# Kernel optimization log

Hardware: AMD Instinct MI355X
Metric: run time of the kernel (lower is better)

Reference implementation:

```python
import jax, jax.numpy as jnp
from jax import lax
import numpy as np

H_FEAT = 14
W_FEAT = 14
BN_EPS = 1e-5
NORM_EPS = 1e-12

def _coord_tensor():
    # Python-2 integer division as in the original repo
    c = np.zeros((H_FEAT * W_FEAT, 2), dtype=np.float32)
    for i in range(H_FEAT * W_FEAT):
        c[i, 0] = (i // W_FEAT - H_FEAT // 2) / (H_FEAT / 2.0)
        c[i, 1] = (i % W_FEAT - W_FEAT // 2) / (W_FEAT / 2.0)
    return jnp.asarray(c.reshape(1, H_FEAT, W_FEAT, 2).transpose(0, 3, 1, 2))  # [1,2,14,14]

def _l2norm(x, axis):
    n = jnp.linalg.norm(x, axis=axis, keepdims=True)
    return x / jnp.maximum(n, NORM_EPS)

def _conv2d(x, w, b, pad):
    y = lax.conv_general_dilated(x, w, (1, 1), [(pad, pad), (pad, pad)],
                                 dimension_numbers=("NCHW", "OIHW", "NCHW"))
    return y + b[None, :, None, None]

def _bn_train(x, g, b):
    m = x.mean(axis=(0, 2, 3), keepdims=True)
    v = x.var(axis=(0, 2, 3), keepdims=True)
    return (x - m) * lax.rsqrt(v + BN_EPS) * g[None, :, None, None] + b[None, :, None, None]

def _lstm_scan(emb, Wih, Whh, bih, bhh):
    # emb: [T, B, 300]; PyTorch gate order i,f,g,o
    Hdim = Whh.shape[1]
    B = emb.shape[1]
    def step(carry, x):
        h, c = carry
        gates = x @ Wih.T + h @ Whh.T + bih + bhh  # [B, 4H]
        i, f, g, o = jnp.split(gates, 4, axis=-1)
        c = jax.nn.sigmoid(f) * c + jax.nn.sigmoid(i) * jnp.tanh(g)
        h = jax.nn.sigmoid(o) * jnp.tanh(c)
        return (h, c), h
    init = (jnp.zeros((B, Hdim), emb.dtype), jnp.zeros((B, Hdim), emb.dtype))
    _, hs = lax.scan(step, init, emb)
    return hs  # [T, B, H]

def _resblock(v, coord, c1w, c1b, c2w, c2b, bng, bnb):
    B = v.shape[0]
    vin = jnp.concatenate([v, jnp.broadcast_to(coord, (B, 2, H_FEAT, W_FEAT))], axis=1)
    v1 = jax.nn.relu(_conv2d(vin, c1w, c1b, 0))
    v2 = jax.nn.relu(_bn_train(_conv2d(v1, c2w, c2b, 1), bng, bnb))
    return v2 + v1

def setup_inputs() -> dict:
    key = jax.random.key(0)
    ks = jax.random.split(key, 24)
    B, T, V, E = 128, 45, 10000, 300
    Hh = 1024
    s = 0.02
    inp = {}
    inp["que"] = jax.random.randint(ks[0], (B, T), 0, V, dtype=jnp.int64)
    inp["img"] = jax.random.normal(ks[1], (B, 1024, H_FEAT, W_FEAT), dtype=jnp.float32)
    inp["lookup"] = s * jax.random.normal(ks[2], (V + 1, E), dtype=jnp.float32)
    inp["Wih_f"] = s * jax.random.normal(ks[3], (4 * Hh, E), dtype=jnp.float32)
    inp["Whh_f"] = s * jax.random.normal(ks[4], (4 * Hh, Hh), dtype=jnp.float32)
    inp["bih_f"] = jnp.zeros((4 * Hh,), jnp.float32)
    inp["bhh_f"] = jnp.zeros((4 * Hh,), jnp.float32)
    inp["Wih_b"] = s * jax.random.normal(ks[5], (4 * Hh, E), dtype=jnp.float32)
    inp["Whh_b"] = s * jax.random.normal(ks[6], (4 * Hh, Hh), dtype=jnp.float32)
    inp["bih_b"] = jnp.zeros((4 * Hh,), jnp.float32)
    inp["bhh_b"] = jnp.zeros((4 * Hh,), jnp.float32)
    inp["conv0_w"] = s * jax.random.normal(ks[7], (128, 1026, 3, 3), dtype=jnp.float32)
    inp["conv0_b"] = jnp.zeros((128,), jnp.float32)
    inp["bn0_g"] = jnp.ones((128,), jnp.float32)
    inp["bn0_b"] = jnp.zeros((128,), jnp.float32)
    inp["r1c1_w"] = s * jax.random.normal(ks[8], (128, 130, 1, 1), dtype=jnp.float32)
    inp["r1c1_b"] = jnp.zeros((128,), jnp.float32)
    inp["r1c2_w"] = s * jax.random.normal(ks[9], (128, 128, 3, 3), dtype=jnp.float32)
    inp["r1c2_b"] = jnp.zeros((128,), jnp.float32)
    inp["r1bn_g"] = jnp.ones((128,), jnp.float32)
    inp["r1bn_b"] = jnp.zeros((128,), jnp.float32)
    inp["r2c1_w"] = s * jax.random.normal(ks[10], (128, 130, 1, 1), dtype=jnp.float32)
    inp["r2c1_b"] = jnp.zeros((128,), jnp.float32)
    inp["r2c2_w"] = s * jax.random.normal(ks[11], (128, 128, 3, 3), dtype=jnp.float32)
    inp["r2c2_b"] = jnp.zeros((128,), jnp.float32)
    inp["r2bn_g"] = jnp.ones((128,), jnp.float32)
    inp["r2bn_b"] = jnp.zeros((128,), jnp.float32)
    return inp

def reference(que, img, lookup, Wih_f, Whh_f, bih_f, bhh_f, Wih_b, Whh_b, bih_b, bhh_b,
              conv0_w, conv0_b, bn0_g, bn0_b,
              r1c1_w, r1c1_b, r1c2_w, r1c2_b, r1bn_g, r1bn_b,
              r2c1_w, r2c1_b, r2c2_w, r2c2_b, r2bn_g, r2bn_b):
    coord = _coord_tensor()
    # ---- encoder (LSTM mode) ----
    emb = lookup[que]                      # [B, T, 300]
    emb = jnp.transpose(emb, (1, 0, 2))    # [T, B, 300]
    h_f = _lstm_scan(emb, Wih_f, Whh_f, bih_f, bhh_f)
    h_b = _lstm_scan(emb[::-1], Wih_b, Whh_b, bih_b, bhh_b)[::-1]
    qenc = _l2norm(jnp.concatenate([h_f, h_b], axis=-1), axis=-1)  # [T, B, 2048]
    enc = qenc[-1]                                                  # [B, 2048]
    # ---- image branch ----
    v = _l2norm(img, axis=1)               # per-pixel L2 norm over 1024 channels
    B = v.shape[0]
    v = jnp.concatenate([v, jnp.broadcast_to(coord, (B, 2, H_FEAT, W_FEAT))], axis=1)
    v = jax.nn.relu(_bn_train(_conv2d(v, conv0_w, conv0_b, 1), bn0_g, bn0_b))
    v = _resblock(v, coord, r1c1_w, r1c1_b, r1c2_w, r1c2_b, r1bn_g, r1bn_b)
    v = _resblock(v, coord, r2c1_w, r2c1_b, r2c2_w, r2c2_b, r2bn_g, r2bn_b)
    return (enc, v)
```

## Files before the change

### kernel.cpp

```cpp
#include <hip/hip_runtime.h>
#include <math.h>

#define BB   128
#define T    45
#define E    300
#define HH   1024
#define G4   4096
#define HW   196
#define NPX  (BB*HW)
#define C0   1026
#define CM   128
#define CR   130
#define TCH  15

static __device__ __forceinline__ float sigm(float x) { return 1.f / (1.f + __expf(-x)); }

__global__ void k_embed(const int* __restrict__ que, const float* __restrict__ lookup,
                        float* __restrict__ emb) {
    int idx = blockIdx.x * 256 + threadIdx.x;
    if (idx >= T * BB * E) return;
    int e = idx % E;
    int n = idx / E;
    int b = n % BB;
    int t = n / BB;
    int q = que[b * T + t];
    emb[idx] = lookup[(size_t)q * E + e];
}

template <int BM, int BN, int TM, int TN>
__global__ __launch_bounds__(256) void k_gemm_nt(
    const float* __restrict__ A, int lda,
    const float* __restrict__ Bw, int ldb,
    const float* __restrict__ add,
    const float* __restrict__ bias,
    float* __restrict__ C, int ldc,
    int M, int N, int K, int relu) {
    constexpr int KT = 16;
    constexpr int TX = BN / TN;
    __shared__ float As[KT][BM + 4];
    __shared__ float Bs[KT][BN + 4];
    const int tid = threadIdx.x;
    const int tx = tid % TX, ty = tid / TX;
    const int r0 = blockIdx.x * BM, c0 = blockIdx.y * BN;
    float acc[TM][TN] = {};
    for (int k0 = 0; k0 < K; k0 += KT) {
#pragma unroll
        for (int l = tid; l < BM * KT; l += 256) {
            int m = l / KT, k = l % KT;
            int gm = r0 + m, gk = k0 + k;
            As[k][m] = (gm < M && gk < K) ? A[(size_t)gm * lda + gk] : 0.f;
        }
#pragma unroll
        for (int l = tid; l < BN * KT; l += 256) {
            int n = l / KT, k = l % KT;
            int gn = c0 + n, gk = k0 + k;
            Bs[k][n] = (gn < N && gk < K) ? Bw[(size_t)gn * ldb + gk] : 0.f;
        }
        __syncthreads();
#pragma unroll
        for (int k = 0; k < KT; ++k) {
            float ar[TM], br[TN];
#pragma unroll
            for (int i = 0; i < TM; ++i) ar[i] = As[k][ty * TM + i];
#pragma unroll
            for (int j = 0; j < TN; ++j) br[j] = Bs[k][tx * TN + j];
#pragma unroll
            for (int i = 0; i < TM; ++i)
#pragma unroll
                for (int j = 0; j < TN; ++j) acc[i][j] += ar[i] * br[j];
        }
        __syncthreads();
    }
#pragma unroll
    for (int i = 0; i < TM; ++i) {
        int gm = r0 + ty * TM + i;
        if (gm >= M) continue;
#pragma unroll
        for (int j = 0; j < TN; ++j) {
            int gn = c0 + tx * TN + j;
            if (gn >= N) continue;
            float v = acc[i][j];
            if (add) v += add[(size_t)gm * ldc + gn];
            if (bias) v += bias[gn];
            if (relu) v = fmaxf(v, 0.f);
            C[(size_t)gm * ldc + gn] = v;
        }
    }
}

__global__ void k_pack_wih(const float* __restrict__ Wih, float* __restrict__ o) {
    int idx = blockIdx.x * 256 + threadIdx.x;
    if (idx >= G4 * E) return;
    int k = idx % E;
    int n = idx / E;
    o[idx] = Wih[(size_t)((n & 3) * HH + (n >> 2)) * E + k];
}
__global__ void k_pack_whh(const float* __restrict__ Whh, float* __restrict__ o) {
    int idx = blockIdx.x * 256 + threadIdx.x;
    if (idx >= G4 * HH) return;
    int k = idx & 1023;
    int n = idx >> 10;
    o[idx] = Whh[(size_t)((n & 3) * HH + (n >> 2)) * HH + k];
}
__global__ void k_pack_b4i(const float* __restrict__ bih, const float* __restrict__ bhh,
                           float* __restrict__ out) {
    int n = blockIdx.x * 256 + threadIdx.x;
    if (n >= G4) return;
    int r = (n & 3) * HH + (n >> 2);
    out[n] = bih[r] + bhh[r];
}
__global__ void k_biasadd(const float* __restrict__ bih, const float* __restrict__ bhh,
                          float* __restrict__ out) {
    int idx = blockIdx.x * 256 + threadIdx.x;
    if (idx < G4) out[idx] = bih[idx] + bhh[idx];
}

__global__ void k_cell_plain(float* __restrict__ h, float* __restrict__ c,
                             const float* __restrict__ gx, int first) {
    int idx = blockIdx.x * 256 + threadIdx.x;
    int b = idx >> 10, j = idx & 1023;
    size_t base = (size_t)b * G4 + j;
    float gi = gx[base], gf = gx[base + HH], gg = gx[base + 2 * HH], go = gx[base + 3 * HH];
    float cp = first ? 0.f : c[idx];
    float cn = sigm(gf) * cp + sigm(gi) * tanhf(gg);
    c[idx] = cn;
    h[idx] = sigm(go) * tanhf(cn);
}

__global__ __launch_bounds__(256) void k_lstm_fused(
    const float* __restrict__ h_in, float* __restrict__ c_io,
    const float* __restrict__ gx,
    const float* __restrict__ Wpk,
    float* __restrict__ h_out, int first) {
    __shared__ float As[16][36];
    __shared__ float Bs[16][68];
    const int tid = threadIdx.x;
    const int tx = tid & 15, ty = tid >> 4;
    const int r0 = blockIdx.x * 32;
    const int c0 = blockIdx.y * 64;
    const int ka = tid & 15, ma = tid >> 4;
    float acc[2][4] = {};

#define LSTM_LD(K0)                                                               \
    {                                                                             \
        int gk = (K0) + ka;                                                       \
        rA0 = h_in[(size_t)(r0 + ma) * HH + gk];                                  \
        rA1 = h_in[(size_t)(r0 + ma + 16) * HH + gk];                             \
        const float* wp = Wpk + (size_t)(c0 + ma) * HH + gk;                      \
        rB0 = wp[0];                                                              \
        rB1 = wp[(size_t)16 * HH];                                                \
        rB2 = wp[(size_t)32 * HH];                                                \
        rB3 = wp[(size_t)48 * HH];                                                \
    }

    if (!first) {
        float rA0, rA1, rB0, rB1, rB2, rB3;
        LSTM_LD(0);
        for (int k0 = 0; k0 < HH; k0 += 16) {
            As[ka][ma] = rA0;
            As[ka][ma + 16] = rA1;
            Bs[ka][ma] = rB0;
            Bs[ka][ma + 16] = rB1;
            Bs[ka][ma + 32] = rB2;
            Bs[ka][ma + 48] = rB3;
            __syncthreads();
            if (k0 + 16 < HH) LSTM_LD(k0 + 16);
#pragma unroll
            for (int k = 0; k < 16; ++k) {
                float a0 = As[k][ty * 2], a1 = As[k][ty * 2 + 1];
                float br[4];
#pragma unroll
                for (int j = 0; j < 4; ++j) br[j] = Bs[k][tx * 4 + j];
#pragma unroll
                for (int j = 0; j < 4; ++j) {
                    acc[0][j] += a0 * br[j];
                    acc[1][j] += a1 * br[j];
                }
            }
            __syncthreads();
        }
    }
#undef LSTM_LD
    const int jj4 = c0 + tx * 4;
    const int u = jj4 >> 2;
#pragma unroll
    for (int i = 0; i < 2; ++i) {
        int b = r0 + ty * 2 + i;
        float4 g4 = *(const float4*)&gx[(size_t)b * G4 + jj4];
        float gi = acc[i][0] + g4.x;
        float gf = acc[i][1] + g4.y;
        float gg = acc[i][2] + g4.z;
        float go = acc[i][3] + g4.w;
        size_t ci = (size_t)b * HH + u;
        float cp = first ? 0.f : c_io[ci];
        float cn = sigm(gf) * cp + sigm(gi) * tanhf(gg);
        c_io[ci] = cn;
        h_out[ci] = sigm(go) * tanhf(cn);
    }
}

__global__ void k_enc(const float* __restrict__ hf, const float* __restrict__ hb,
                      float* __restrict__ out) {
    int b = blockIdx.x;
    int tid = threadIdx.x;
    float vals[8];
    float ss = 0.f;
#pragma unroll
    for (int i = 0; i < 8; ++i) {
        int j = i * 256 + tid;
        float v = (j < HH) ? hf[(size_t)b * HH + j] : hb[(size_t)b * HH + (j - HH)];
        vals[i] = v;
        ss += v * v;
    }
    __shared__ float red[256];
    red[tid] = ss;
    __syncthreads();
    for (int s = 128; s > 0; s >>= 1) {
        if (tid < s) red[tid] += red[tid + s];
        __syncthreads();
    }
    float scale = 1.f / fmaxf(sqrtf(red[0]), 1e-12f);
#pragma unroll
    for (int i = 0; i < 8; ++i) out[(size_t)b * 2048 + i * 256 + tid] = vals[i] * scale;
}

__global__ void k_pixssq(const float* __restrict__ img, float* __restrict__ ssq) {
    int b = blockIdx.x >> 4;
    int cc = (blockIdx.x & 15) * 64;
    int p = threadIdx.x;
    if (p >= HW) return;
    const float* base = img + ((size_t)b * 1024 + cc) * HW + p;
    float acc = 0.f;
#pragma unroll 4
    for (int c = 0; c < 64; ++c) {
        float v = base[(size_t)c * HW];
        acc += v * v;
    }
    atomicAdd(&ssq[b * HW + p], acc);
}

__global__ void k_invn(float* __restrict__ ssq) {
    int i = blockIdx.x * 256 + threadIdx.x;
    if (i >= NPX) return;
    ssq[i] = 1.f / fmaxf(sqrtf(ssq[i]), 1e-12f);
}

__global__ void k_packB0(const float* __restrict__ w, float* __restrict__ o) {
    int idx = blockIdx.x * 256 + threadIdx.x;
    if (idx >= 8 * 9 * 1040 * 16) return;
    int oi = idx & 15;
    int r = idx >> 4;
    int c = r % 1040;
    int gt = r / 1040;
    int tap = gt % 9, ocg = gt / 9;
    o[idx] = (c < C0) ? w[((size_t)(ocg * 16 + oi) * C0 + c) * 9 + tap] : 0.f;
}
__global__ void k_packBpm(const float* __restrict__ w, float* __restrict__ o) {
    int idx = blockIdx.x * 256 + threadIdx.x;
    if (idx >= 8 * 9 * 128 * 16) return;
    int oi = idx & 15;
    int r = idx >> 4;
    int c = r % 128;
    int gt = r / 128;
    int tap = gt % 9, ocg = gt / 9;
    o[idx] = w[((size_t)(ocg * 16 + oi) * 128 + c) * 9 + tap];
}

static __device__ __forceinline__ void conv_swizzle(int id, int& g, int& ocg, int& z) {
    int x = id & 7, q = id >> 3;
    int cb;
    if (q < 192) { g = ((q >> 4) << 3) + x; cb = q & 15; }
    else { int r = ((q - 192) << 3) + x; g = 96 + (r >> 4); cb = r & 15; }
    ocg = cb >> 1;
    z = cb & 1;
}

__global__ __launch_bounds__(256) void k_conv0(const float* __restrict__ img,
                                               const float* __restrict__ invn,
                                               const float* __restrict__ wpk,
                                               const float* __restrict__ bias,
                                               float* __restrict__ outParts) {
    __shared__ float As[289][20];
    const int tid = threadIdx.x;
    int g, ocg, z;
    conv_swizzle(blockIdx.x, g, ocg, z);
    const int kbeg = z ? 528 : 0;
    const int kend = z ? 1040 : 528;
    float* out = outParts + (size_t)z * NPX * CM;
    const int P0 = g * 256;
    const int gpix = P0 + tid;
    const int p = gpix % HW;
    const int y = p / 14, x = p % 14;
    float acc[16] = {};
    if (tid < 16) As[288][tid] = 0.f;
    for (int k0 = kbeg; k0 < kend; k0 += 16) {
        __syncthreads();
        for (int l = tid; l < 288 * 16; l += 256) {
            int s = l >> 4, k = l & 15;
            int gp = P0 - 16 + s;
            float v = 0.f;
            if (gp >= 0 && gp < NPX) {
                int gk = k0 + k;
                int pp = gp % HW;
                int bi = gp / HW;
                if (gk < 1024) v = img[((size_t)bi * 1024 + gk) * HW + pp] * invn[gp];
                else if (gk == 1024) v = (float)(pp / 14 - 7) * (1.f / 7.f);
                else if (gk == 1025) v = (float)(pp % 14 - 7) * (1.f / 7.f);
            }
            As[s][k] = v;
        }
        __syncthreads();
        for (int tap = 0; tap < 9; ++tap) {
            const int ky = tap / 3 - 1, kx = tap % 3 - 1;
            const int yy = y + ky, xx = x + kx;
            const int of = ((unsigned)yy < 14u && (unsigned)xx < 14u)
                               ? (tid + 16 + ky * 14 + kx) : 288;
            const float4* __restrict__ wq =
                (const float4*)wpk + ((size_t)(ocg * 9 + tap) * 1040 + k0) * 4;
            for (int kq = 0; kq < 4; ++kq) {
                float4 a4 = *(const float4*)&As[of][kq * 4];
                float av[4] = {a4.x, a4.y, a4.z, a4.w};
#pragma unroll
                for (int kk = 0; kk < 4; ++kk) {
                    float a = av[kk];
                    float4 w0 = wq[0], w1 = wq[1], w2 = wq[2], w3 = wq[3];
                    wq += 4;
                    acc[0]  += a * w0.x;  acc[1]  += a * w0.y;
                    acc[2]  += a * w0.z;  acc[3]  += a * w0.w;
                    acc[4]  += a * w1.x;  acc[5]  += a * w1.y;
                    acc[6]  += a * w1.z;  acc[7]  += a * w1.w;
                    acc[8]  += a * w2.x;  acc[9]  += a * w2.y;
                    acc[10] += a * w2.z;  acc[11] += a * w2.w;
                    acc[12] += a * w3.x;  acc[13] += a * w3.y;
                    acc[14] += a * w3.z;  acc[15] += a * w3.w;
                }
            }
        }
    }
    float* op = out + (size_t)gpix * CM + ocg * 16;
    const float* bp = bias + ocg * 16;
#pragma unroll
    for (int qq = 0; qq < 4; ++qq) {
        float4 r;
        r.x = acc[qq * 4 + 0] + (z ? 0.f : bp[qq * 4 + 0]);
        r.y = acc[qq * 4 + 1] + (z ? 0.f : bp[qq * 4 + 1]);
        r.z = acc[qq * 4 + 2] + (z ? 0.f : bp[qq * 4 + 2]);
        r.w = acc[qq * 4 + 3] + (z ? 0.f : bp[qq * 4 + 3]);
        *(float4*)&op[qq * 4] = r;
    }
}

__global__ __launch_bounds__(256) void k_conv_pm(const float* __restrict__ vin,
                                                 const float* __restrict__ wpk,
                                                 const float* __restrict__ bias,
                                                 float* __restrict__ outParts) {
    __shared__ float As[289][20];
    const int tid = threadIdx.x;
    int g, ocg, z;
    conv_swizzle(blockIdx.x, g, ocg, z);
    const int kbeg = z * 64;
    float* out = outParts + (size_t)z * NPX * CM;
    const int P0 = g * 256;
    const int gpix = P0 + tid;
    const int p = gpix % HW;
    const int y = p / 14, x = p % 14;
    float acc[16] = {};
    if (tid < 16) As[288][tid] = 0.f;
    for (int k0 = kbeg; k0 < kbeg + 64; k0 += 16) {
        __syncthreads();
        for (int l = tid; l < 288 * 4; l += 256) {
            int s = l >> 2, kq = l & 3;
            int gp = P0 - 16 + s;
            float4 v;
            v.x = v.y = v.z = v.w = 0.f;
            if (gp >= 0 && gp < NPX) v = *(const float4*)&vin[(size_t)gp * CM + k0 + kq * 4];
            *(float4*)&As[s][kq * 4] = v;
        }
        __syncthreads();
        for (int tap = 0; tap < 9; ++tap) {
            const int ky = tap / 3 - 1, kx = tap % 3 - 1;
            const int yy = y + ky, xx = x + kx;
            const int of = ((unsigned)yy < 14u && (unsigned)xx < 14u)
                               ? (tid + 16 + ky * 14 + kx) : 288;
            const float4* __restrict__ wq =
                (const float4*)wpk + ((size_t)(ocg * 9 + tap) * 128 + k0) * 4;
            for (int kq = 0; kq < 4; ++kq) {
                float4 a4 = *(const float4*)&As[of][kq * 4];
                float av[4] = {a4.x, a4.y, a4.z, a4.w};
#pragma unroll
                for (int kk = 0; kk < 4; ++kk) {
                    float a = av[kk];
                    float4 w0 = wq[0], w1 = wq[1], w2 = wq[2], w3 = wq[3];
                    wq += 4;
                    acc[0]  += a * w0.x;  acc[1]  += a * w0.y;
                    acc[2]  += a * w0.z;  acc[3]  += a * w0.w;
                    acc[4]  += a * w1.x;  acc[5]  += a * w1.y;
                    acc[6]  += a * w1.z;  acc[7]  += a * w1.w;
                    acc[8]  += a * w2.x;  acc[9]  += a * w2.y;
                    acc[10] += a * w2.z;  acc[11] += a * w2.w;
                    acc[12] += a * w3.x;  acc[13] += a * w3.y;
                    acc[14] += a * w3.z;  acc[15] += a * w3.w;
                }
            }
        }
    }
    float* op = out + (size_t)gpix * CM + ocg * 16;
    const float* bp = bias + ocg * 16;
#pragma unroll
    for (int qq = 0; qq < 4; ++qq) {
        float4 r;
        r.x = acc[qq * 4 + 0] + (z ? 0.f : bp[qq * 4 + 0]);
        r.y = acc[qq * 4 + 1] + (z ? 0.f : bp[qq * 4 + 1]);
        r.z = acc[qq * 4 + 2] + (z ? 0.f : bp[qq * 4 + 2]);
        r.w = acc[qq * 4 + 3] + (z ? 0.f : bp[qq * 4 + 3]);
        *(float4*)&op[qq * 4] = r;
    }
}

__global__ void k_bnstats(const float* __restrict__ xa, const float* __restrict__ xb,
                          float* __restrict__ stats) {
    int r0 = blockIdx.x * 224;
    int c = threadIdx.x & 127, rh = threadIdx.x >> 7;
    float s = 0.f, ss = 0.f;
    for (int r = r0 + rh; r < r0 + 224; r += 2) {
        float v = xa[(size_t)r * CM + c] + xb[(size_t)r * CM + c];
        s += v;
        ss += v * v;
    }
    __shared__ float rs[256], rss[256];
    rs[threadIdx.x] = s;
    rss[threadIdx.x] = ss;
    __syncthreads();
    if (threadIdx.x < 128) {
        s = rs[threadIdx.x] + rs[threadIdx.x + 128];
        ss = rss[threadIdx.x] + rss[threadIdx.x + 128];
        atomicAdd(&stats[c], s);
        atomicAdd(&stats[128 + c], ss);
    }
}

__global__ void k_bnfinal(const float* __restrict__ stats, const float* __restrict__ g,
                          const float* __restrict__ b, float* __restrict__ scsh) {
    int c = threadIdx.x;
    if (c >= 128) return;
    float mean = stats[c] / (float)NPX;
    float var = stats[128 + c] / (float)NPX - mean * mean;
    float sc = g[c] * rsqrtf(var + 1e-5f);
    scsh[c] = sc;
    scsh[128 + c] = b[c] - mean * sc;
}

__global__ void k_apply_cat(const float* __restrict__ xa, const float* __restrict__ xb,
                            const float* __restrict__ scsh,
                            const float* __restrict__ addv, float* __restrict__ vinr) {
    int idx = blockIdx.x * 256 + threadIdx.x;
    if (idx >= NPX * CM) return;
    int c = idx & 127;
    int p = idx >> 7;
    float v = fmaxf((xa[idx] + xb[idx]) * scsh[c] + scsh[128 + c], 0.f);
    if (addv) v += addv[idx];
    vinr[(size_t)p * CR + c] = v;
}

__global__ void k_coords_r(float* __restrict__ vinr) {
    int p = blockIdx.x * 256 + threadIdx.x;
    if (p >= NPX) return;
    int pp = p % HW;
    int y = pp / 14, x = pp % 14;
    vinr[(size_t)p * CR + 128] = (float)(y - 7) * (1.f / 7.f);
    vinr[(size_t)p * CR + 129] = (float)(x - 7) * (1.f / 7.f);
}

__global__ void k_final(const float* __restrict__ xa, const float* __restrict__ xb,
                        const float* __restrict__ scsh,
                        const float* __restrict__ addv, float* __restrict__ outv) {
    int idx = blockIdx.x * 256 + threadIdx.x;
    if (idx >= NPX * CM) return;
    int p = idx % HW;
    int o = (idx / HW) & 127;
    int b = idx / (HW * CM);
    size_t pm = ((size_t)b * HW + p) * CM + o;
    outv[idx] = fmaxf((xa[pm] + xb[pm]) * scsh[o] + scsh[128 + o], 0.f) + addv[pm];
}

extern "C" void kernel_launch(void* const* d_in, const int* in_sizes, int n_in,
                              void* d_out, int out_size, void* d_ws, size_t ws_size,
                              hipStream_t stream) {
    const int* que = (const int*)d_in[0];
    const float* img = (const float*)d_in[1];
    const float* lookup = (const float*)d_in[2];
    const float* Wih_f = (const float*)d_in[3];
    const float* Whh_f = (const float*)d_in[4];
    const float* bih_f = (const float*)d_in[5];
    const float* bhh_f = (const float*)d_in[6];
    const float* Wih_b = (const float*)d_in[7];
    const float* bih_b = (const float*)d_in[9];
    const float* bhh_b = (const float*)d_in[10];
    const float* conv0_w = (const float*)d_in[11];
    const float* conv0_b = (const float*)d_in[12];
    const float* bn0_g = (const float*)d_in[13];
    const float* bn0_b = (const float*)d_in[14];
    const float* r1c1_w = (const float*)d_in[15];
    const float* r1c1_b = (const float*)d_in[16];
    const float* r1c2_w = (const float*)d_in[17];
    const float* r1c2_b = (const float*)d_in[18];
    const float* r1bn_g = (const float*)d_in[19];
    const float* r1bn_b = (const float*)d_in[20];
    const float* r2c1_w = (const float*)d_in[21];
    const float* r2c1_b = (const float*)d_in[22];
    const float* r2c2_w = (const float*)d_in[23];
    const float* r2c2_b = (const float*)d_in[24];
    const float* r2bn_g = (const float*)d_in[25];
    const float* r2bn_b = (const float*)d_in[26];
    float* out = (float*)d_out;

    float* ws = (float*)d_ws;
    float* emb = ws;
    float* Xg = emb + 1728000;
    float* WihPk = Xg + 7864320;
    float* WhhPk = WihPk + 1228800;
    float* b4i = WhhPk + 4194304;
    float* b4b = b4i + 4096;
    float* Xb = b4b + 4096;
    float* hA = Xb + 524288;
    float* hB = hA + 131072;
    float* cbuf = hB + 131072;
    float* hbb = cbuf + 131072;
    size_t lstm_end = (size_t)(hbb + 131072 - ws);
    float* invn = ws;
    float* wpk0 = invn + 25088;
    float* wpk1 = wpk0 + 1198080;
    float* wpk2 = wpk1 + 147456;
    float* xa = wpk2 + 147456;
    float* xb = xa + 3211264;
    float* vinr = xb + 3211264;
    float* v1 = vinr + 3261440;
    float* stats = v1 + 3211264;
    float* scsh = stats + 256;
    size_t img_end = (size_t)(scsh + 256 - ws);
    size_t need = (lstm_end > img_end ? lstm_end : img_end) * 4;
    if (ws_size < need) return;

    auto cdiv = [](int a, int b) { return (a + b - 1) / b; };
    const size_t BG = (size_t)BB * G4;

    k_embed<<<cdiv(T * BB * E, 256), 256, 0, stream>>>(que, lookup, emb);
    k_pack_wih<<<cdiv(G4 * E, 256), 256, 0, stream>>>(Wih_f, WihPk);
    k_pack_whh<<<cdiv(G4 * HH, 256), 256, 0, stream>>>(Whh_f, WhhPk);
    k_pack_b4i<<<16, 256, 0, stream>>>(bih_f, bhh_f, b4i);
    k_biasadd<<<16, 256, 0, stream>>>(bih_b, bhh_b, b4b);
    k_gemm_nt<64, 64, 4, 4><<<dim3(2, 64), 256, 0, stream>>>(
        emb + (size_t)(T - 1) * BB * E, E, Wih_b, E, nullptr, b4b, Xb, G4, BB, G4, E, 0);
    k_cell_plain<<<512, 256, 0, stream>>>(hbb, cbuf, Xb, 1);
    float* hp = hA;
    float* hq = hB;
    float* hlast = hA;
    for (int ch = 0; ch < 3; ++ch) {
        int t0 = ch * TCH;
        k_gemm_nt<64, 64, 4, 4><<<dim3(30, 64), 256, 0, stream>>>(
            emb + (size_t)t0 * BB * E, E, WihPk, E, nullptr, b4i, Xg, G4,
            TCH * BB, G4, E, 0);
        for (int s = 0; s < TCH; ++s) {
            int t = t0 + s;
            k_lstm_fused<<<dim3(4, 64), 256, 0, stream>>>(
                hq, cbuf, Xg + (size_t)s * BG, WhhPk, hp, (t == 0) ? 1 : 0);
            hlast = hp;
            float* tmp = hp; hp = hq; hq = tmp;
        }
    }
    k_enc<<<128, 256, 0, stream>>>(hlast, hbb, out);

    hipMemsetAsync(invn, 0, NPX * 4, stream);
    k_pixssq<<<BB * 16, 256, 0, stream>>>(img, invn);
    k_invn<<<cdiv(NPX, 256), 256, 0, stream>>>(invn);
    k_packB0<<<cdiv(8 * 9 * 1040 * 16, 256), 256, 0, stream>>>(conv0_w, wpk0);
    k_packBpm<<<cdiv(8 * 9 * 128 * 16, 256), 256, 0, stream>>>(r1c2_w, wpk1);
    k_packBpm<<<cdiv(8 * 9 * 128 * 16, 256), 256, 0, stream>>>(r2c2_w, wpk2);

    k_conv0<<<1568, 256, 0, stream>>>(img, invn, wpk0, conv0_b, xa);
    hipMemsetAsync(stats, 0, 256 * 4, stream);
    k_bnstats<<<112, 256, 0, stream>>>(xa, xb, stats);
    k_bnfinal<<<1, 128, 0, stream>>>(stats, bn0_g, bn0_b, scsh);
    k_apply_cat<<<cdiv(NPX * CM, 256), 256, 0, stream>>>(xa, xb, scsh, nullptr, vinr);
    k_coords_r<<<cdiv(NPX, 256), 256, 0, stream>>>(vinr);

    k_gemm_nt<64, 64, 4, 4><<<dim3(392, 2), 256, 0, stream>>>(
        vinr, CR, r1c1_w, CR, nullptr, r1c1_b, v1, CM, NPX, CM, CR, 1);
    k_conv_pm<<<1568, 256, 0, stream>>>(v1, wpk1, r1c2_b, xa);
    hipMemsetAsync(stats, 0, 256 * 4, stream);
    k_bnstats<<<112, 256, 0, stream>>>(xa, xb, stats);
    k_bnfinal<<<1, 128, 0, stream>>>(stats, r1bn_g, r1bn_b, scsh);
    k_apply_cat<<<cdiv(NPX * CM, 256), 256, 0, stream>>>(xa, xb, scsh, v1, vinr);

    k_gemm_nt<64, 64, 4, 4><<<dim3(392, 2), 256, 0, stream>>>(
        vinr, CR, r2c1_w, CR, nullptr, r2c1_b, v1, CM, NPX, CM, CR, 1);
    k_conv_pm<<<1568, 256, 0, stream>>>(v1, wpk2, r2c2_b, xa);
    hipMemsetAsync(stats, 0, 256 * 4, stream);
    k_bnstats<<<112, 256, 0, stream>>>(xa, xb, stats);
    k_bnfinal<<<1, 128, 0, stream>>>(stats, r2bn_g, r2bn_b, scsh);
    k_final<<<cdiv(NPX * CM, 256), 256, 0, stream>>>(xa, xb, scsh, v1, out + (size_t)BB * 2048);
}
```

Measured before the change: 4.254 ms.

## Compute two pixels per thread in 3x3 conv kernels to reuse weight loads

Each thread in the conv0 and residual 3x3 conv kernels now accumulates two pixels, with 512 pixels per block instead of 256. The grid is halved and uses a new block swizzle. Every weight float4 loaded from global memory now feeds twice as many FMAs, which cuts weight-read traffic per output. conv0 also precomputes per-thread image pointers and inverse norms and stages the image slab with strided loads. The costs are double the accumulator registers, a larger shared tile with an 18-float padded stride read as float2, fewer blocks per launch, and possible occupancy loss.

```diff
diff --git a/kernel.cpp b/kernel.cpp
--- a/kernel.cpp
+++ b/kernel.cpp
@@ -266,11 +266,10 @@
     o[idx] = w[((size_t)(ocg * 16 + oi) * 128 + c) * 9 + tap];
 }
 
-static __device__ __forceinline__ void conv_swizzle(int id, int& g, int& ocg, int& z) {
-    int x = id & 7, q = id >> 3;
-    int cb;
-    if (q < 192) { g = ((q >> 4) << 3) + x; cb = q & 15; }
-    else { int r = ((q - 192) << 3) + x; g = 96 + (r >> 4); cb = r & 15; }
+static __device__ __forceinline__ void conv_swz784(int id, int& g, int& ocg, int& z) {
+    int s2 = (id & 7) * 98 + (id >> 3);
+    g = s2 >> 4;
+    int cb = s2 & 15;
     ocg = cb >> 1;
     z = cb & 1;
 }
@@ -280,73 +279,122 @@
                                                const float* __restrict__ wpk,
                                                const float* __restrict__ bias,
                                                float* __restrict__ outParts) {
-    __shared__ float As[289][20];
+    __shared__ float As[545][18];
     const int tid = threadIdx.x;
     int g, ocg, z;
-    conv_swizzle(blockIdx.x, g, ocg, z);
+    conv_swz784(blockIdx.x, g, ocg, z);
     const int kbeg = z ? 528 : 0;
     const int kend = z ? 1040 : 528;
     float* out = outParts + (size_t)z * NPX * CM;
-    const int P0 = g * 256;
-    const int gpix = P0 + tid;
-    const int p = gpix % HW;
-    const int y = p / 14, x = p % 14;
-    float acc[16] = {};
-    if (tid < 16) As[288][tid] = 0.f;
+    const int P0 = g * 512;
+    const int gp1 = P0 + tid;
+    const int gp2 = gp1 + 256;
+    const int p1 = gp1 % HW, p2 = gp2 % HW;
+    const int y1 = p1 / 14, x1 = p1 % 14;
+    const int y2 = p2 / 14, x2 = p2 % 14;
+
+    const float* sptr[3];
+    float sinv[3], scy[3], scx[3];
+#pragma unroll
+    for (int j = 0; j < 3; ++j) {
+        int s = tid + j * 256;
+        int gp = P0 - 16 + s;
+        bool ok = (s <= 542) && (gp >= 0) && (gp < NPX);
+        int gpc = ok ? gp : 0;
+        int pp = gpc % HW;
+        int bi = gpc / HW;
+        sptr[j] = img + ((size_t)bi * 1024) * HW + pp;
+        sinv[j] = ok ? invn[gpc] : 0.f;
+        scy[j] = ok ? (float)(pp / 14 - 7) * (1.f / 7.f) : 0.f;
+        scx[j] = ok ? (float)(pp % 14 - 7) * (1.f / 7.f) : 0.f;
+    }
+
+    float acc0[16] = {};
+    float acc1[16] = {};
     for (int k0 = kbeg; k0 < kend; k0 += 16) {
         __syncthreads();
-        for (int l = tid; l < 288 * 16; l += 256) {
-            int s = l >> 4, k = l & 15;
-            int gp = P0 - 16 + s;
-            float v = 0.f;
-            if (gp >= 0 && gp < NPX) {
-                int gk = k0 + k;
-                int pp = gp % HW;
-                int bi = gp / HW;
-                if (gk < 1024) v = img[((size_t)bi * 1024 + gk) * HW + pp] * invn[gp];
-                else if (gk == 1024) v = (float)(pp / 14 - 7) * (1.f / 7.f);
-                else if (gk == 1025) v = (float)(pp % 14 - 7) * (1.f / 7.f);
+        if (k0 < 1024) {
+#pragma unroll
+            for (int j = 0; j < 3; ++j) {
+                int s = tid + j * 256;
+                if (j < 2 || s < 545) {
+                    const float* pbase = sptr[j] + (size_t)k0 * HW;
+                    float inv = sinv[j];
+#pragma unroll
+                    for (int k = 0; k < 16; ++k) As[s][k] = pbase[(size_t)k * HW] * inv;
+                }
             }
-            As[s][k] = v;
+        } else {
+#pragma unroll
+            for (int j = 0; j < 3; ++j) {
+                int s = tid + j * 256;
+                if (j < 2 || s < 545) {
+                    As[s][0] = scy[j];
+                    As[s][1] = scx[j];
+#pragma unroll
+                    for (int k = 2; k < 16; ++k) As[s][k] = 0.f;
+                }
+            }
         }
         __syncthreads();
         for (int tap = 0; tap < 9; ++tap) {
             const int ky = tap / 3 - 1, kx = tap % 3 - 1;
-            const int yy = y + ky, xx = x + kx;
-            const int of = ((unsigned)yy < 14u && (unsigned)xx < 14u)
-                               ? (tid + 16 + ky * 14 + kx) : 288;
+            const int d = ky * 14 + kx;
+            const int of1 = ((unsigned)(y1 + ky) < 14u && (unsigned)(x1 + kx) < 14u)
+                                ? (tid + 16 + d) : 544;
+            const int of2 = ((unsigned)(y2 + ky) < 14u && (unsigned)(x2 + kx) < 14u)
+                                ? (tid + 272 + d) : 544;
             const float4* __restrict__ wq =
                 (const float4*)wpk + ((size_t)(ocg * 9 + tap) * 1040 + k0) * 4;
+#pragma unroll
             for (int kq = 0; kq < 4; ++kq) {
-                float4 a4 = *(const float4*)&As[of][kq * 4];
-                float av[4] = {a4.x, a4.y, a4.z, a4.w};
+                float2 a01 = *(const float2*)&As[of1][kq * 4];
+                float2 a23 = *(const float2*)&As[of1][kq * 4 + 2];
+                float2 b01 = *(const float2*)&As[of2][kq * 4];
+                float2 b23 = *(const float2*)&As[of2][kq * 4 + 2];
+                float av[4] = {a01.x, a01.y, a23.x, a23.y};
+                float bv[4] = {b01.x, b01.y, b23.x, b23.y};
 #pragma unroll
                 for (int kk = 0; kk < 4; ++kk) {
-                    float a = av[kk];
+                    float a = av[kk], b = bv[kk];
                     float4 w0 = wq[0], w1 = wq[1], w2 = wq[2], w3 = wq[3];
                     wq += 4;
-                    acc[0]  += a * w0.x;  acc[1]  += a * w0.y;
-                    acc[2]  += a * w0.z;  acc[3]  += a * w0.w;
-                    acc[4]  += a * w1.x;  acc[5]  += a * w1.y;
-                    acc[6]  += a * w1.z;  acc[7]  += a * w1.w;
-                    acc[8]  += a * w2.x;  acc[9]  += a * w2.y;
-                    acc[10] += a * w2.z;  acc[11] += a * w2.w;
-                    acc[12] += a * w3.x;  acc[13] += a * w3.y;
-                    acc[14] += a * w3.z;  acc[15] += a * w3.w;
+                    acc0[0]  += a * w0.x;  acc1[0]  += b * w0.x;
+                    acc0[1]  += a * w0.y;  acc1[1]  += b * w0.y;
+                    acc0[2]  += a * w0.z;  acc1[2]  += b * w0.z;
+                    acc0[3]  += a * w0.w;  acc1[3]  += b * w0.w;
+                    acc0[4]  += a * w1.x;  acc1[4]  += b * w1.x;
+                    acc0[5]  += a * w1.y;  acc1[5]  += b * w1.y;
+                    acc0[6]  += a * w1.z;  acc1[6]  += b * w1.z;
+                    acc0[7]  += a * w1.w;  acc1[7]  += b * w1.w;
+                    acc0[8]  += a * w2.x;  acc1[8]  += b * w2.x;
+                    acc0[9]  += a * w2.y;  acc1[9]  += b * w2.y;
+                    acc0[10] += a * w2.z;  acc1[10] += b * w2.z;
+                    acc0[11] += a * w2.w;  acc1[11] += b * w2.w;
+                    acc0[12] += a * w3.x;  acc1[12] += b * w3.x;
+                    acc0[13] += a * w3.y;  acc1[13] += b * w3.y;
+                    acc0[14] += a * w3.z;  acc1[14] += b * w3.z;
+                    acc0[15] += a * w3.w;  acc1[15] += b * w3.w;
                 }
             }
         }
     }
-    float* op = out + (size_t)gpix * CM + ocg * 16;
     const float* bp = bias + ocg * 16;
+    float* op1 = out + (size_t)gp1 * CM + ocg * 16;
+    float* op2 = out + (size_t)gp2 * CM + ocg * 16;
 #pragma unroll
     for (int qq = 0; qq < 4; ++qq) {
-        float4 r;
-        r.x = acc[qq * 4 + 0] + (z ? 0.f : bp[qq * 4 + 0]);
-        r.y = acc[qq * 4 + 1] + (z ? 0.f : bp[qq * 4 + 1]);
-        r.z = acc[qq * 4 + 2] + (z ? 0.f : bp[qq * 4 + 2]);
-        r.w = acc[qq * 4 + 3] + (z ? 0.f : bp[qq * 4 + 3]);
-        *(float4*)&op[qq * 4] = r;
+        float b0 = z ? 0.f : bp[qq * 4 + 0];
+        float b1 = z ? 0.f : bp[qq * 4 + 1];
+        float b2 = z ? 0.f : bp[qq * 4 + 2];
+        float b3 = z ? 0.f : bp[qq * 4 + 3];
+        float4 r0, r1;
+        r0.x = acc0[qq * 4 + 0] + b0;  r1.x = acc1[qq * 4 + 0] + b0;
+        r0.y = acc0[qq * 4 + 1] + b1;  r1.y = acc1[qq * 4 + 1] + b1;
+        r0.z = acc0[qq * 4 + 2] + b2;  r1.z = acc1[qq * 4 + 2] + b2;
+        r0.w = acc0[qq * 4 + 3] + b3;  r1.w = acc1[qq * 4 + 3] + b3;
+        *(float4*)&op1[qq * 4] = r0;
+        *(float4*)&op2[qq * 4] = r1;
     }
 }
 
@@ -354,66 +402,93 @@
                                                  const float* __restrict__ wpk,
                                                  const float* __restrict__ bias,
                                                  float* __restrict__ outParts) {
-    __shared__ float As[289][20];
+    __shared__ float As[545][18];
     const int tid = threadIdx.x;
     int g, ocg, z;
-    conv_swizzle(blockIdx.x, g, ocg, z);
+    conv_swz784(blockIdx.x, g, ocg, z);
     const int kbeg = z * 64;
     float* out = outParts + (size_t)z * NPX * CM;
-    const int P0 = g * 256;
-    const int gpix = P0 + tid;
-    const int p = gpix % HW;
-    const int y = p / 14, x = p % 14;
-    float acc[16] = {};
-    if (tid < 16) As[288][tid] = 0.f;
+    const int P0 = g * 512;
+    const int gp1 = P0 + tid;
+    const int gp2 = gp1 + 256;
+    const int p1 = gp1 % HW, p2 = gp2 % HW;
+    const int y1 = p1 / 14, x1 = p1 % 14;
+    const int y2 = p2 / 14, x2 = p2 % 14;
+    float acc0[16] = {};
+    float acc1[16] = {};
     for (int k0 = kbeg; k0 < kbeg + 64; k0 += 16) {
         __syncthreads();
-        for (int l = tid; l < 288 * 4; l += 256) {
+        for (int l = tid; l < 545 * 4; l += 256) {
             int s = l >> 2, kq = l & 3;
             int gp = P0 - 16 + s;
             float4 v;
             v.x = v.y = v.z = v.w = 0.f;
-            if (gp >= 0 && gp < NPX) v = *(const float4*)&vin[(size_t)gp * CM + k0 + kq * 4];
-            *(float4*)&As[s][kq * 4] = v;
+            if (s <= 542 && gp >= 0 && gp < NPX)
+                v = *(const float4*)&vin[(size_t)gp * CM + k0 + kq * 4];
+            As[s][kq * 4 + 0] = v.x;
+            As[s][kq * 4 + 1] = v.y;
+            As[s][kq * 4 + 2] = v.z;
+            As[s][kq * 4 + 3] = v.w;
         }
         __syncthreads();
         for (int tap = 0; tap < 9; ++tap) {
             const int ky = tap / 3 - 1, kx = tap % 3 - 1;
-            const int yy = y + ky, xx = x + kx;
-            const int of = ((unsigned)yy < 14u && (unsigned)xx < 14u)
-                               ? (tid + 16 + ky * 14 + kx) : 288;
+            const int d = ky * 14 + kx;
+            const int of1 = ((unsigned)(y1 + ky) < 14u && (unsigned)(x1 + kx) < 14u)
+                                ? (tid + 16 + d) : 544;
+            const int of2 = ((unsigned)(y2 + ky) < 14u && (unsigned)(x2 + kx) < 14u)
+                                ? (tid + 272 + d) : 544;
             const float4* __restrict__ wq =
                 (const float4*)wpk + ((size_t)(ocg * 9 + tap) * 128 + k0) * 4;
+#pragma unroll
             for (int kq = 0; kq < 4; ++kq) {
-                float4 a4 = *(const float4*)&As[of][kq * 4];
-                float av[4] = {a4.x, a4.y, a4.z, a4.w};
+                float2 a01 = *(const float2*)&As[of1][kq * 4];
+                float2 a23 = *(const float2*)&As[of1][kq * 4 + 2];
+                float2 b01 = *(const float2*)&As[of2][kq * 4];
+                float2 b23 = *(const float2*)&As[of2][kq * 4 + 2];
+                float av[4] = {a01.x, a01.y, a23.x, a23.y};
+                float bv[4] = {b01.x, b01.y, b23.x, b23.y};
 #pragma unroll
                 for (int kk = 0; kk < 4; ++kk) {
-                    float a = av[kk];
+                    float a = av[kk], b = bv[kk];
                     float4 w0 = wq[0], w1 = wq[1], w2 = wq[2], w3 = wq[3];
                     wq += 4;
-                    acc[0]  += a * w0.x;  acc[1]  += a * w0.y;
-                    acc[2]  += a * w0.z;  acc[3]  += a * w0.w;
-                    acc[4]  += a * w1.x;  acc[5]  += a * w1.y;
-                    acc[6]  += a * w1.z;  acc[7]  += a * w1.w;
-                    acc[8]  += a * w2.x;  acc[9]  += a * w2.y;
-                    acc[10] += a * w2.z;  acc[11] += a * w2.w;
-                    acc[12] += a * w3.x;  acc[13] += a * w3.y;
-                    acc[14] += a * w3.z;  acc[15] += a * w3.w;
+                    acc0[0]  += a * w0.x;  acc1[0]  += b * w0.x;
+                    acc0[1]  += a * w0.y;  acc1[1]  += b * w0.y;
+                    acc0[2]  += a * w0.z;  acc1[2]  += b * w0.z;
+                    acc0[3]  += a * w0.w;  acc1[3]  += b * w0.w;
+                    acc0[4]  += a * w1.x;  acc1[4]  += b * w1.x;
+                    acc0[5]  += a * w1.y;  acc1[5]  += b * w1.y;
+                    acc0[6]  += a * w1.z;  acc1[6]  += b * w1.z;
+                    acc0[7]  += a * w1.w;  acc1[7]  += b * w1.w;
+                    acc0[8]  += a * w2.x;  acc1[8]  += b * w2.x;
+                    acc0[9]  += a * w2.y;  acc1[9]  += b * w2.y;
+                    acc0[10] += a * w2.z;  acc1[10] += b * w2.z;
+                    acc0[11] += a * w2.w;  acc1[11] += b * w2.w;
+                    acc0[12] += a * w3.x;  acc1[12] += b * w3.x;
+                    acc0[13] += a * w3.y;  acc1[13] += b * w3.y;
+                    acc0[14] += a * w3.z;  acc1[14] += b * w3.z;
+                    acc0[15] += a * w3.w;  acc1[15] += b * w3.w;
                 }
             }
         }
     }
-    float* op = out + (size_t)gpix * CM + ocg * 16;
     const float* bp = bias + ocg * 16;
+    float* op1 = out + (size_t)gp1 * CM + ocg * 16;
+    float* op2 = out + (size_t)gp2 * CM + ocg * 16;
 #pragma unroll
     for (int qq = 0; qq < 4; ++qq) {
-        float4 r;
-        r.x = acc[qq * 4 + 0] + (z ? 0.f : bp[qq * 4 + 0]);
-        r.y = acc[qq * 4 + 1] + (z ? 0.f : bp[qq * 4 + 1]);
-        r.z = acc[qq * 4 + 2] + (z ? 0.f : bp[qq * 4 + 2]);
-        r.w = acc[qq * 4 + 3] + (z ? 0.f : bp[qq * 4 + 3]);
-        *(float4*)&op[qq * 4] = r;
+        float b0 = z ? 0.f : bp[qq * 4 + 0];
+        float b1 = z ? 0.f : bp[qq * 4 + 1];
+        float b2 = z ? 0.f : bp[qq * 4 + 2];
+        float b3 = z ? 0.f : bp[qq * 4 + 3];
+        float4 r0, r1;
+        r0.x = acc0[qq * 4 + 0] + b0;  r1.x = acc1[qq * 4 + 0] + b0;
+        r0.y = acc0[qq * 4 + 1] + b1;  r1.y = acc1[qq * 4 + 1] + b1;
+        r0.z = acc0[qq * 4 + 2] + b2;  r1.z = acc1[qq * 4 + 2] + b2;
+        r0.w = acc0[qq * 4 + 3] + b3;  r1.w = acc1[qq * 4 + 3] + b3;
+        *(float4*)&op1[qq * 4] = r0;
+        *(float4*)&op2[qq * 4] = r1;
     }
 }
 
@@ -577,7 +652,7 @@
     k_packBpm<<<cdiv(8 * 9 * 128 * 16, 256), 256, 0, stream>>>(r1c2_w, wpk1);
     k_packBpm<<<cdiv(8 * 9 * 128 * 16, 256), 256, 0, stream>>>(r2c2_w, wpk2);
 
-    k_conv0<<<1568, 256, 0, stream>>>(img, invn, wpk0, conv0_b, xa);
+    k_conv0<<<784, 256, 0, stream>>>(img, invn, wpk0, conv0_b, xa);
     hipMemsetAsync(stats, 0, 256 * 4, stream);
     k_bnstats<<<112, 256, 0, stream>>>(xa, xb, stats);
     k_bnfinal<<<1, 128, 0, stream>>>(stats, bn0_g, bn0_b, scsh);
@@ -586,7 +661,7 @@
 
     k_gemm_nt<64, 64, 4, 4><<<dim3(392, 2), 256, 0, stream>>>(
         vinr, CR, r1c1_w, CR, nullptr, r1c1_b, v1, CM, NPX, CM, CR, 1);
-    k_conv_pm<<<1568, 256, 0, stream>>>(v1, wpk1, r1c2_b, xa);
+    k_conv_pm<<<784, 256, 0, stream>>>(v1, wpk1, r1c2_b, xa);
     hipMemsetAsync(stats, 0, 256 * 4, stream);
     k_bnstats<<<112, 256, 0, stream>>>(xa, xb, stats);
     k_bnfinal<<<1, 128, 0, stream>>>(stats, r1bn_g, r1bn_b, scsh);
@@ -594,7 +669,7 @@
 
     k_gemm_nt<64, 64, 4, 4><<<dim3(392, 2), 256, 0, stream>>>(
         vinr, CR, r2c1_w, CR, nullptr, r2c1_b, v1, CM, NPX, CM, CR, 1);
-    k_conv_pm<<<1568, 256, 0, stream>>>(v1, wpk2, r2c2_b, xa);
+    k_conv_pm<<<784, 256, 0, stream>>>(v1, wpk2, r2c2_b, xa);
     hipMemsetAsync(stats, 0, 256 * 4, stream);
     k_bnstats<<<112, 256, 0, stream>>>(xa, xb, stats);
     k_bnfinal<<<1, 128, 0, stream>>>(stats, r2bn_g, r2bn_b, scsh);
```

Measured after the change: 3.988 ms. -6.2%, faster.
